# Optimization experiments

Measured on AMD Instinct MI355X. Metric: run time of the kernel, lower is better.

Reference implementation:

```python
import jax, jax.numpy as jnp
import numpy as np

B, NQ, NK, QS, KS, H, VD = 16, 64, 512, 256, 256, 256, 256


def setup_inputs() -> dict:
    key = jax.random.key(0)
    k1, k2, k3, k4, k5, k6, k7 = jax.random.split(key, 7)
    return {
        "queries": jax.random.normal(k1, (B, NQ, QS), dtype=jnp.float32),
        "keys": jax.random.normal(k2, (B, NK, KS), dtype=jnp.float32),
        "values": jax.random.normal(k3, (B, NK, VD), dtype=jnp.float32),
        "valid_lens": jax.random.randint(k4, (B,), 1, NK + 1, dtype=jnp.int32),
        # learned params (nn.Linear with bias=False): W_q [QS,H], W_k [KS,H], w_v [H]
        "W_q": jax.random.normal(k5, (QS, H), dtype=jnp.float32) / np.sqrt(QS),
        "W_k": jax.random.normal(k6, (KS, H), dtype=jnp.float32) / np.sqrt(KS),
        "w_v": jax.random.normal(k7, (H,), dtype=jnp.float32) / np.sqrt(H),
    }


def reference(queries, keys, values, valid_lens, W_q, W_k, w_v):
    # project: q [B,nq,H], k [B,nk,H]
    q = jnp.einsum("bqd,dh->bqh", queries, W_q)
    k = jnp.einsum("bkd,dh->bkh", keys, W_k)
    # broadcast-add -> tanh -> score reduction via w_v: [B,nq,nk]
    features = jnp.tanh(q[:, :, None, :] + k[:, None, :, :])  # [B,nq,nk,H]
    scores = jnp.einsum("bqkh,h->bqk", features, w_v)
    # masked softmax over keys (positions >= valid_len masked out)
    mask = jnp.arange(scores.shape[-1])[None, None, :] < valid_lens[:, None, None]
    scores = jnp.where(mask, scores, -1e6)
    attn = jax.nn.softmax(scores, axis=-1)
    # weighted sum of values (dropout p=0 / eval mode => identity)
    return jnp.einsum("bqk,bkv->bqv", attn, values)
```

## Files before the change

kernel.cpp:

```cpp
#include <hip/hip_runtime.h>
#include <hip/hip_bf16.h>

#define BB 16
#define NQ 64
#define NK 512
#define HD 256

typedef __attribute__((ext_vector_type(8))) short short8;
typedef __attribute__((ext_vector_type(4))) float f32x4;

__device__ __forceinline__ ushort bf16_rne(float v) {
    unsigned u = __float_as_uint(v);
    return (ushort)((u + 0x7FFFu + ((u >> 16) & 1u)) >> 16);
}
__device__ __forceinline__ float bf16_to_f(ushort h) {
    return __uint_as_float(((unsigned)h) << 16);
}

__global__ __launch_bounds__(512, 4) void proj_all(
    const float* __restrict__ queries, const float* __restrict__ keys,
    const float* __restrict__ W_q, const float* __restrict__ W_k,
    float* __restrict__ qp, float* __restrict__ kp, float scale)
{
    __shared__ ushort AsH[64 * 64], AsL[64 * 64];
    __shared__ ushort WtH[64 * 64], WtL[64 * 64];

    const float* A; const float* W; float* C; int rows0;
    const int bx = blockIdx.x;
    if (bx < 16) { A = queries; W = W_q; C = qp; rows0 = bx * 64; }
    else         { A = keys;    W = W_k; C = kp; rows0 = (bx - 16) * 64; }
    const int cols0 = blockIdx.y * 64;

    const int t = threadIdx.x, lane = t & 63, wave = t >> 6;
    const int quad = lane >> 4, l15 = lane & 15;
    const int sr = t >> 3, sc = t & 7;
    const int wn = t & 63, wkc = t >> 6;
    const int mw = wave & 3, nw = wave >> 2;

    f32x4 acc[2];
    acc[0] = (f32x4){0.f, 0.f, 0.f, 0.f};
    acc[1] = (f32x4){0.f, 0.f, 0.f, 0.f};

    for (int k0 = 0; k0 < 256; k0 += 64) {
        const float* arow = &A[(size_t)(rows0 + sr) * 256 + k0 + sc * 8];
        float4 a0 = *(const float4*)&arow[0];
        float4 a1 = *(const float4*)&arow[4];
        float wr[8];
        #pragma unroll
        for (int j = 0; j < 8; ++j)
            wr[j] = W[(size_t)(k0 + wkc * 8 + j) * 256 + cols0 + wn];

        __syncthreads();

        {
            float av[8] = {a0.x, a0.y, a0.z, a0.w, a1.x, a1.y, a1.z, a1.w};
            short8 ah, al;
            #pragma unroll
            for (int e = 0; e < 8; ++e) {
                ushort h = bf16_rne(av[e]);
                ah[e] = (short)h;
                al[e] = (short)bf16_rne(av[e] - bf16_to_f(h));
            }
            int slot = sr * 8 + (sc ^ (sr & 7));
            *(short8*)&AsH[slot * 8] = ah;
            *(short8*)&AsL[slot * 8] = al;
        }
        {
            short8 h8, l8;
            #pragma unroll
            for (int j = 0; j < 8; ++j) {
                ushort h = bf16_rne(wr[j]);
                h8[j] = (short)h;
                l8[j] = (short)bf16_rne(wr[j] - bf16_to_f(h));
            }
            int slot = wn * 8 + (wkc ^ (wn & 7));
            *(short8*)&WtH[slot * 8] = h8;
            *(short8*)&WtL[slot * 8] = l8;
        }
        __syncthreads();

        #pragma unroll
        for (int ks = 0; ks < 2; ++ks) {
            const int c = ks * 4 + quad;
            short8 aH, aL, bH[2], bL[2];
            {
                int r = mw * 16 + l15;
                int slot = r * 8 + (c ^ (r & 7));
                aH = *(const short8*)&AsH[slot * 8];
                aL = *(const short8*)&AsL[slot * 8];
            }
            #pragma unroll
            for (int ns = 0; ns < 2; ++ns) {
                int n = nw * 32 + ns * 16 + l15;
                int slot = n * 8 + (c ^ (n & 7));
                bH[ns] = *(const short8*)&WtH[slot * 8];
                bL[ns] = *(const short8*)&WtL[slot * 8];
            }
            #pragma unroll
            for (int ns = 0; ns < 2; ++ns)
                acc[ns] = __builtin_amdgcn_mfma_f32_16x16x32_bf16(aH, bH[ns], acc[ns], 0, 0, 0);
            #pragma unroll
            for (int ns = 0; ns < 2; ++ns)
                acc[ns] = __builtin_amdgcn_mfma_f32_16x16x32_bf16(aL, bH[ns], acc[ns], 0, 0, 0);
            #pragma unroll
            for (int ns = 0; ns < 2; ++ns)
                acc[ns] = __builtin_amdgcn_mfma_f32_16x16x32_bf16(aH, bL[ns], acc[ns], 0, 0, 0);
        }
    }

    const int rbase = rows0 + mw * 16 + quad * 4;
    #pragma unroll
    for (int ns = 0; ns < 2; ++ns) {
        int col = cols0 + nw * 32 + ns * 16 + l15;
        #pragma unroll
        for (int r = 0; r < 4; ++r)
            C[(size_t)(rbase + r) * 256 + col] = acc[ns][r] * scale;
    }
}

__global__ __launch_bounds__(512, 4) void score_pv_seg4(
    const float* __restrict__ qp,
    const float* __restrict__ kp,
    const float* __restrict__ values,
    const int*   __restrict__ vlens,
    const float* __restrict__ w_v,
    float* __restrict__ pO,
    float* __restrict__ pM,
    float* __restrict__ pL)
{
    __shared__ float eq[8][260];
    __shared__ float wv[HD];
    __shared__ float Ps[8][68];
    __shared__ float part[4][2][260];

    const int b   = blockIdx.x & 15;
    const int qt  = blockIdx.x >> 4;
    const int seg = blockIdx.y;
    const int vl  = vlens[b];
    if (seg * 64 >= vl) return;

    const int t = threadIdx.x, lane = t & 63, wave = t >> 6;

    const float* qsrc = qp + ((size_t)b * NQ + qt * 8) * HD;
    {
        int row = t >> 6, c4 = (t & 63) * 4;
        float4 v = *(const float4*)&qsrc[(size_t)row * HD + c4];
        eq[row][c4 + 0] = __builtin_amdgcn_exp2f(v.x);
        eq[row][c4 + 1] = __builtin_amdgcn_exp2f(v.y);
        eq[row][c4 + 2] = __builtin_amdgcn_exp2f(v.z);
        eq[row][c4 + 3] = __builtin_amdgcn_exp2f(v.w);
    }
    if (t < 64) *(float4*)&wv[t * 4] = *(const float4*)&w_v[t * 4];
    __syncthreads();

    float Wsum;
    {
        float ws = wv[lane] + wv[lane + 64] + wv[lane + 128] + wv[lane + 192];
        #pragma unroll
        for (int off = 32; off; off >>= 1) ws += __shfl_xor(ws, off);
        Wsum = ws;
    }

    const int key = wave * 8 + (lane >> 3);
    const int ch  = lane & 7;
    const int kg  = seg * 64 + key;
    const float* krow = kp + ((size_t)b * NK + kg) * HD + ch * 4;

    float4 kk[8];
    #pragma unroll
    for (int j = 0; j < 8; ++j) kk[j] = *(const float4*)&krow[j * 32];

    float s[8] = {0.f, 0.f, 0.f, 0.f, 0.f, 0.f, 0.f, 0.f};
    #pragma unroll
    for (int j = 0; j < 8; ++j) {
        const int h = j * 32 + ch * 4;
        float4 w4 = *(const float4*)&wv[h];
        float ek0 = __builtin_amdgcn_exp2f(kk[j].x);
        float ek1 = __builtin_amdgcn_exp2f(kk[j].y);
        float ek2 = __builtin_amdgcn_exp2f(kk[j].z);
        float ek3 = __builtin_amdgcn_exp2f(kk[j].w);
        #pragma unroll
        for (int qi = 0; qi < 8; ++qi) {
            float4 q4 = *(const float4*)&eq[qi][h];
            float t0 = fmaf(w4.x, __builtin_amdgcn_rcpf(fmaf(q4.x, ek0, 1.f)), s[qi]);
            t0 = fmaf(w4.y, __builtin_amdgcn_rcpf(fmaf(q4.y, ek1, 1.f)), t0);
            t0 = fmaf(w4.z, __builtin_amdgcn_rcpf(fmaf(q4.z, ek2, 1.f)), t0);
            s[qi] = fmaf(w4.w, __builtin_amdgcn_rcpf(fmaf(q4.w, ek3, 1.f)), t0);
        }
    }
    #pragma unroll
    for (int qi = 0; qi < 8; ++qi) {
        s[qi] += __shfl_xor(s[qi], 1);
        s[qi] += __shfl_xor(s[qi], 2);
        s[qi] += __shfl_xor(s[qi], 4);
    }
    if (ch == 0) {
        const bool masked = (kg >= vl);
        #pragma unroll
        for (int qi = 0; qi < 8; ++qi)
            Ps[qi][key] = masked ? -1e6f : fmaf(-2.f, s[qi], Wsum);
    }
    __syncthreads();

    const float L2E = 1.4426950408889634f;
    {
        float sv = Ps[wave][lane];
        float m = sv;
        #pragma unroll
        for (int off = 32; off; off >>= 1) m = fmaxf(m, __shfl_xor(m, off));
        float e = __builtin_amdgcn_exp2f((sv - m) * L2E);
        float l = e;
        #pragma unroll
        for (int off = 32; off; off >>= 1) l += __shfl_xor(l, off);
        Ps[wave][lane] = e;
        if (lane == 0) {
            size_t mi = (((size_t)(b * 8 + qt) * 8 + seg)) * 8 + wave;
            pM[mi] = m;
            pL[mi] = l;
        }
    }
    __syncthreads();

    const int r0 = (wave & 3) * 2, r1 = r0 + 1;
    const int kb = (wave >> 2) * 32;
    f32x4 acc0 = (f32x4){0.f, 0.f, 0.f, 0.f};
    f32x4 acc1 = (f32x4){0.f, 0.f, 0.f, 0.f};
    const float* vbase = values + ((size_t)b * NK + seg * 64 + kb) * HD;
    #pragma unroll 2
    for (int i0 = 0; i0 < 32; i0 += 4) {
        float4 v[4];
        #pragma unroll
        for (int u = 0; u < 4; ++u)
            v[u] = *(const float4*)&vbase[(size_t)(i0 + u) * HD + lane * 4];
        #pragma unroll
        for (int u = 0; u < 4; ++u) {
            float p0 = Ps[r0][kb + i0 + u];
            float p1 = Ps[r1][kb + i0 + u];
            acc0[0] = fmaf(p0, v[u].x, acc0[0]);
            acc0[1] = fmaf(p0, v[u].y, acc0[1]);
            acc0[2] = fmaf(p0, v[u].z, acc0[2]);
            acc0[3] = fmaf(p0, v[u].w, acc0[3]);
            acc1[0] = fmaf(p1, v[u].x, acc1[0]);
            acc1[1] = fmaf(p1, v[u].y, acc1[1]);
            acc1[2] = fmaf(p1, v[u].z, acc1[2]);
            acc1[3] = fmaf(p1, v[u].w, acc1[3]);
        }
    }
    if (wave >= 4) {
        *(f32x4*)&part[wave - 4][0][lane * 4] = acc0;
        *(f32x4*)&part[wave - 4][1][lane * 4] = acc1;
    }
    __syncthreads();
    if (wave < 4) {
        float4 q0 = *(const float4*)&part[wave][0][lane * 4];
        float4 q1 = *(const float4*)&part[wave][1][lane * 4];
        acc0[0] += q0.x; acc0[1] += q0.y; acc0[2] += q0.z; acc0[3] += q0.w;
        acc1[0] += q1.x; acc1[1] += q1.y; acc1[2] += q1.z; acc1[3] += q1.w;
        const size_t ob = (((size_t)(b * 8 + qt) * 8 + seg)) * 8 * 256;
        *(f32x4*)&pO[ob + (size_t)r0 * 256 + lane * 4] = acc0;
        *(f32x4*)&pO[ob + (size_t)r1 * 256 + lane * 4] = acc1;
    }
}

__global__ __launch_bounds__(256) void combine_seg2(
    const float* __restrict__ pO, const float* __restrict__ pM,
    const float* __restrict__ pL, const int* __restrict__ vlens,
    float* __restrict__ out)
{
    const int b  = blockIdx.x >> 6;
    const int q  = blockIdx.x & 63;
    const int t  = threadIdx.x;
    const int vl = vlens[b];
    const int nc = (vl + 63) >> 6;
    const int qt = q >> 3, qi = q & 7;
    const float L2E = 1.4426950408889634f;

    const size_t base = (size_t)(b * 8 + qt) * 8;

    float mi[8], li[8];
    float m = -3e38f;
    #pragma unroll
    for (int i = 0; i < 8; ++i) {
        if (i < nc) {
            mi[i] = pM[(base + i) * 8 + qi];
            li[i] = pL[(base + i) * 8 + qi];
            m = fmaxf(m, mi[i]);
        }
    }
    float L = 0.f, wi[8];
    #pragma unroll
    for (int i = 0; i < 8; ++i) {
        if (i < nc) {
            wi[i] = __builtin_amdgcn_exp2f((mi[i] - m) * L2E);
            L = fmaf(li[i], wi[i], L);
        }
    }
    float acc = 0.f;
    #pragma unroll
    for (int i = 0; i < 8; ++i) {
        if (i < nc) acc = fmaf(wi[i], pO[((base + i) * 8 + qi) * 256 + t], acc);
    }
    out[((size_t)(b * 64 + q)) * 256 + t] = acc * __builtin_amdgcn_rcpf(L);
}

extern "C" void kernel_launch(void* const* d_in, const int* in_sizes, int n_in,
                              void* d_out, int out_size, void* d_ws, size_t ws_size,
                              hipStream_t stream) {
    const float* queries = (const float*)d_in[0];
    const float* keys    = (const float*)d_in[1];
    const float* values  = (const float*)d_in[2];
    const int*   vlens   = (const int*)d_in[3];
    const float* W_q     = (const float*)d_in[4];
    const float* W_k     = (const float*)d_in[5];
    const float* w_v     = (const float*)d_in[6];
    float* out = (float*)d_out;

    float* kp = (float*)d_ws;
    float* qp = kp + (size_t)BB * NK * HD;
    float* pO = qp + (size_t)BB * NQ * HD;
    float* pM = pO + (size_t)BB * 8 * 8 * 8 * 256;
    float* pL = pM + (size_t)BB * 8 * 8 * 8;

    const float SC = 2.885390081777927f;

    proj_all<<<dim3(144, 4), 512, 0, stream>>>(queries, keys, W_q, W_k,
                                               qp, kp, SC);
    score_pv_seg4<<<dim3(128, 8), 512, 0, stream>>>(qp, kp, values, vlens, w_v,
                                                    pO, pM, pL);
    combine_seg2<<<dim3(BB * NQ), 256, 0, stream>>>(pO, pM, pL, vlens, out);
}
```

Baseline: 115.0 us.

## Double-buffer LDS tiles in projection GEMM to overlap loads with MFMA

The projection kernel now keeps two LDS buffers for the split-bf16 A and W tiles. It prefetches the next k-slice from global memory into registers while the MFMAs run on the current buffer, then converts and stores that slice into the other buffer. This removes one barrier per iteration and hides global load latency behind compute. In exchange it doubles LDS use to 64KB per block, which may reduce occupancy, and it only affects the projection kernel, which is a small part of total time.

```diff
diff --git a/kernel.cpp b/kernel.cpp
--- a/kernel.cpp
+++ b/kernel.cpp
@@ -22,8 +22,8 @@
     const float* __restrict__ W_q, const float* __restrict__ W_k,
     float* __restrict__ qp, float* __restrict__ kp, float scale)
 {
-    __shared__ ushort AsH[64 * 64], AsL[64 * 64];
-    __shared__ ushort WtH[64 * 64], WtL[64 * 64];
+    __shared__ ushort AsH[2][64 * 64], AsL[2][64 * 64];
+    __shared__ ushort WtH[2][64 * 64], WtL[2][64 * 64];
 
     const float* A; const float* W; float* C; int rows0;
     const int bx = blockIdx.x;
@@ -41,43 +41,57 @@
     acc[0] = (f32x4){0.f, 0.f, 0.f, 0.f};
     acc[1] = (f32x4){0.f, 0.f, 0.f, 0.f};
 
-    for (int k0 = 0; k0 < 256; k0 += 64) {
-        const float* arow = &A[(size_t)(rows0 + sr) * 256 + k0 + sc * 8];
-        float4 a0 = *(const float4*)&arow[0];
-        float4 a1 = *(const float4*)&arow[4];
-        float wr[8];
+    float4 a0, a1;
+    float wr[8];
+
+    auto cvst = [&](int bsel) {
+        float av[8] = {a0.x, a0.y, a0.z, a0.w, a1.x, a1.y, a1.z, a1.w};
+        short8 ah, al;
+        #pragma unroll
+        for (int e = 0; e < 8; ++e) {
+            ushort h = bf16_rne(av[e]);
+            ah[e] = (short)h;
+            al[e] = (short)bf16_rne(av[e] - bf16_to_f(h));
+        }
+        int slotA = sr * 8 + (sc ^ (sr & 7));
+        *(short8*)&AsH[bsel][slotA * 8] = ah;
+        *(short8*)&AsL[bsel][slotA * 8] = al;
+
+        short8 h8, l8;
+        #pragma unroll
+        for (int j = 0; j < 8; ++j) {
+            ushort h = bf16_rne(wr[j]);
+            h8[j] = (short)h;
+            l8[j] = (short)bf16_rne(wr[j] - bf16_to_f(h));
+        }
+        int slotW = wn * 8 + (wkc ^ (wn & 7));
+        *(short8*)&WtH[bsel][slotW * 8] = h8;
+        *(short8*)&WtL[bsel][slotW * 8] = l8;
+    };
+
+    {
+        const float* arow = &A[(size_t)(rows0 + sr) * 256 + sc * 8];
+        a0 = *(const float4*)&arow[0];
+        a1 = *(const float4*)&arow[4];
         #pragma unroll
         for (int j = 0; j < 8; ++j)
-            wr[j] = W[(size_t)(k0 + wkc * 8 + j) * 256 + cols0 + wn];
-
-        __syncthreads();
-
-        {
-            float av[8] = {a0.x, a0.y, a0.z, a0.w, a1.x, a1.y, a1.z, a1.w};
-            short8 ah, al;
-            #pragma unroll
-            for (int e = 0; e < 8; ++e) {
-                ushort h = bf16_rne(av[e]);
-                ah[e] = (short)h;
-                al[e] = (short)bf16_rne(av[e] - bf16_to_f(h));
-            }
-            int slot = sr * 8 + (sc ^ (sr & 7));
-            *(short8*)&AsH[slot * 8] = ah;
-            *(short8*)&AsL[slot * 8] = al;
-        }
-        {
-            short8 h8, l8;
-            #pragma unroll
-            for (int j = 0; j < 8; ++j) {
-                ushort h = bf16_rne(wr[j]);
-                h8[j] = (short)h;
-                l8[j] = (short)bf16_rne(wr[j] - bf16_to_f(h));
-            }
-            int slot = wn * 8 + (wkc ^ (wn & 7));
-            *(short8*)&WtH[slot * 8] = h8;
-            *(short8*)&WtL[slot * 8] = l8;
-        }
-        __syncthreads();
+            wr[j] = W[(size_t)(wkc * 8 + j) * 256 + cols0 + wn];
+    }
+    cvst(0);
+    __syncthreads();
+
+    for (int it = 0; it < 4; ++it) {
+        const int buf = it & 1;
+
+        if (it < 3) {
+            const int kn = (it + 1) * 64;
+            const float* arow = &A[(size_t)(rows0 + sr) * 256 + kn + sc * 8];
+            a0 = *(const float4*)&arow[0];
+            a1 = *(const float4*)&arow[4];
+            #pragma unroll
+            for (int j = 0; j < 8; ++j)
+                wr[j] = W[(size_t)(kn + wkc * 8 + j) * 256 + cols0 + wn];
+        }
 
         #pragma unroll
         for (int ks = 0; ks < 2; ++ks) {
@@ -86,15 +100,15 @@
             {
                 int r = mw * 16 + l15;
                 int slot = r * 8 + (c ^ (r & 7));
-                aH = *(const short8*)&AsH[slot * 8];
-                aL = *(const short8*)&AsL[slot * 8];
+                aH = *(const short8*)&AsH[buf][slot * 8];
+                aL = *(const short8*)&AsL[buf][slot * 8];
             }
             #pragma unroll
             for (int ns = 0; ns < 2; ++ns) {
                 int n = nw * 32 + ns * 16 + l15;
                 int slot = n * 8 + (c ^ (n & 7));
-                bH[ns] = *(const short8*)&WtH[slot * 8];
-                bL[ns] = *(const short8*)&WtL[slot * 8];
+                bH[ns] = *(const short8*)&WtH[buf][slot * 8];
+                bL[ns] = *(const short8*)&WtL[buf][slot * 8];
             }
             #pragma unroll
             for (int ns = 0; ns < 2; ++ns)
@@ -105,6 +119,11 @@
             #pragma unroll
             for (int ns = 0; ns < 2; ++ns)
                 acc[ns] = __builtin_amdgcn_mfma_f32_16x16x32_bf16(aH, bL[ns], acc[ns], 0, 0, 0);
+        }
+
+        if (it < 3) {
+            cvst(buf ^ 1);
+            __syncthreads();
         }
     }
 
```

Result: no change. 115.1 us (+0.1%).
